# Performance work log

Hardware: AMD Instinct MI355X
Metric: run time of the kernel (lower is better)

## Reference

```python
import jax, jax.numpy as jnp
import numpy as np

IN_F = 128
OUT_F = 128
SCALE = float(np.sqrt(OUT_F))

def swish(x):
    return x * jax.nn.sigmoid(x)

def setup_inputs() -> dict:
    key = jax.random.key(0)
    ks = jax.random.split(key, 10)
    B, A = 4, 4096
    s = 1.0 / np.sqrt(IN_F)
    return {
        "x": jax.random.normal(ks[0], (B, A, IN_F), dtype=jnp.float32),
        "connectivity": jax.random.normal(ks[1], (B, A, A), dtype=jnp.float32),
        "Wq": jax.random.uniform(ks[2], (IN_F, OUT_F), jnp.float32, -s, s),
        "Wk": jax.random.uniform(ks[3], (IN_F, OUT_F), jnp.float32, -s, s),
        "Wv": jax.random.uniform(ks[4], (IN_F, OUT_F), jnp.float32, -s, s),
        "W1": jax.random.uniform(ks[5], (OUT_F, OUT_F), jnp.float32, -s, s),
        "b1": jnp.zeros((OUT_F,), jnp.float32),
        "W2": jax.random.uniform(ks[6], (OUT_F, OUT_F), jnp.float32, -s, s),
        "b2": jnp.zeros((OUT_F,), jnp.float32),
        "gamma": jnp.ones((OUT_F,), jnp.float32),
        "beta": jnp.zeros((OUT_F,), jnp.float32),
    }

def reference(x, connectivity, Wq, Wk, Wv, W1, b1, W2, b2, gamma, beta):
    # Q,K,V projections (no bias): [B,A,D]
    Q = jnp.einsum('bah,hd->bad', x, Wq)
    K = jnp.einsum('bah,hd->bad', x, Wk)
    V = jnp.einsum('bah,hd->bad', x, Wv)
    # dense all-pairs scores with additive connectivity bias: [B,A,A]
    scores = jnp.einsum('bqd,bkd->bqk', Q, K) / SCALE + connectivity
    alpha = jax.nn.softmax(scores, axis=-1)
    # dropout p=0.0 / eval mode -> identity
    H = jnp.einsum('bqk,bkd->bqd', alpha, V)
    # Swish-MLP tail
    h = swish(H)
    h = h @ W1 + b1
    h = swish(h)
    h = h @ W2 + b2
    # LayerNorm over last dim (eps=1e-5 as torch default)
    mu = jnp.mean(h, axis=-1, keepdims=True)
    var = jnp.var(h, axis=-1, keepdims=True)
    return (h - mu) * jax.lax.rsqrt(var + 1e-5) * gamma + beta
```

## Files before the change

### kernel.cpp

```cpp
#include <hip/hip_runtime.h>

#define L2E 1.44269504088896340736f
#define INV_SCALE 0.08838834764831845f

typedef _Float16 half8 __attribute__((ext_vector_type(8)));
typedef _Float16 half4 __attribute__((ext_vector_type(4)));
typedef float f32x4 __attribute__((ext_vector_type(4)));

__device__ __forceinline__ float exp2_fast(float x) {
#if __has_builtin(__builtin_amdgcn_exp2f)
  return __builtin_amdgcn_exp2f(x);
#else
  return exp2f(x);
#endif
}

__device__ __forceinline__ f32x4 mfma16(half8 a, half8 b, f32x4 c) {
  return __builtin_amdgcn_mfma_f32_16x16x32_f16(a, b, c, 0, 0, 0);
}

__device__ __forceinline__ void gload16(const void* g, void* l) {
  __builtin_amdgcn_global_load_lds(
      (const __attribute__((address_space(1))) void*)g,
      (__attribute__((address_space(3))) void*)l, 16, 0, 0);
}

__device__ __forceinline__ float swish_f(float v) {
  return v / (1.f + exp2_fast(-L2E * v));
}

template <int CTRL>
__device__ __forceinline__ float dppmov(float x) {
  int xi = __builtin_bit_cast(int, x);
  int r = __builtin_amdgcn_update_dpp(xi, xi, CTRL, 0xf, 0xf, false);
  return __builtin_bit_cast(float, r);
}
__device__ __forceinline__ float red16_sum(float x) {
  x += dppmov<0xB1>(x);
  x += dppmov<0x4E>(x);
  x += dppmov<0x141>(x);
  x += dppmov<0x140>(x);
  return x;
}

__global__ __launch_bounds__(256) void prep_kernel(
    const float* __restrict__ Wq, const float* __restrict__ Wk,
    const float* __restrict__ Wv, const float* __restrict__ W1,
    const float* __restrict__ W2, _Float16* __restrict__ Wf) {
  const int g = blockIdx.x * 256 + threadIdx.x;
  const int mat = g >> 11, rem = g & 2047;
  const int f = rem >> 6, lane = rem & 63;
  const int n = (f >> 2) * 16 + (lane & 15);
  const int k0 = (f & 3) * 32 + (lane >> 4) * 8;
  const float* W = (mat == 0) ? Wq : (mat == 1) ? Wk : (mat == 2) ? Wv
                   : (mat == 3) ? W1 : W2;
  half8 h;
#pragma unroll
  for (int j = 0; j < 8; ++j) h[j] = (_Float16)W[(k0 + j) * 128 + n];
  *(half8*)(Wf + (size_t)g * 8) = h;
}

__global__ __launch_bounds__(256) void kv_kernel(
    const float* __restrict__ x, const _Float16* __restrict__ Wf,
    _Float16* __restrict__ Kg, _Float16* __restrict__ Vg) {
  __shared__ __align__(16) _Float16 sc[64 * 136];
  const int tid = threadIdx.x;
  const int w = tid >> 6, lane = tid & 63;
  const int n16 = lane & 15, quad = lane >> 4;
  const int blk = blockIdx.x;

  half8 xf[4];
  {
    const float* xr = x + (size_t)(blk * 64 + w * 16 + n16) * 128 + quad * 8;
#pragma unroll
    for (int kc = 0; kc < 4; ++kc) {
      float4 a = *(const float4*)(xr + kc * 32);
      float4 b = *(const float4*)(xr + kc * 32 + 4);
      half8 h;
      h[0] = (_Float16)a.x; h[1] = (_Float16)a.y;
      h[2] = (_Float16)a.z; h[3] = (_Float16)a.w;
      h[4] = (_Float16)b.x; h[5] = (_Float16)b.y;
      h[6] = (_Float16)b.z; h[7] = (_Float16)b.w;
      xf[kc] = h;
    }
  }

  for (int mat = 0; mat < 2; ++mat) {
    f32x4 acc[8];
#pragma unroll
    for (int ct = 0; ct < 8; ++ct) acc[ct] = f32x4{0.f, 0.f, 0.f, 0.f};
#pragma unroll
    for (int ct = 0; ct < 8; ++ct)
#pragma unroll
      for (int kc = 0; kc < 4; ++kc) {
        half8 wf = *(const half8*)(Wf +
            ((size_t)((mat + 1) * 32 + ct * 4 + kc) * 64 + lane) * 8);
        acc[ct] = mfma16(xf[kc], wf, acc[ct]);
      }
#pragma unroll
    for (int ct = 0; ct < 8; ++ct)
#pragma unroll
      for (int r = 0; r < 4; ++r)
        sc[(w * 16 + quad * 4 + r) * 136 + ct * 16 + n16] = (_Float16)acc[ct][r];
    __syncthreads();

    if (mat == 0) {
#pragma unroll
      for (int i = 0; i < 4; ++i) {
        const int c = tid + 256 * i;
        const int ln = c & 63, kc = (c >> 6) & 3, ct = (c >> 8) & 1, tl = (c >> 9) & 1;
        half8 v = *(const half8*)&sc[(tl * 32 + ct * 16 + (ln & 15)) * 136 +
                                     kc * 32 + (ln >> 4) * 8];
        *(half8*)(Kg + ((((size_t)(blk * 2 + tl)) * 2 + ct) * 4 + kc) * 512 + ln * 8) = v;
      }
    } else {
#pragma unroll
      for (int i = 0; i < 4; ++i) {
        const int c = tid + 256 * i;
        const int ln = c & 63, dt = (c >> 6) & 7, tl = (c >> 9) & 1;
        const int q2 = ln >> 4, nn = ln & 15;
        half8 v;
#pragma unroll
        for (int j = 0; j < 8; ++j)
          v[j] = sc[(tl * 32 + q2 * 8 + j) * 136 + dt * 16 + nn];
        *(half8*)(Vg + (((size_t)(blk * 2 + tl)) * 8 + dt) * 512 + ln * 8) = v;
      }
    }
    __syncthreads();
  }
}

template <int NW>
__global__ __launch_bounds__(NW * 64) void flash_kernel(
    const float* __restrict__ x, const float* __restrict__ conn,
    const _Float16* __restrict__ Wf,
    const _Float16* __restrict__ Kg, const _Float16* __restrict__ Vg,
    _Float16* __restrict__ Og, float2* __restrict__ Ml,
    int nsplit, int nt) {
  __shared__ __align__(16) _Float16 kb[2][4096];
  __shared__ __align__(16) _Float16 vb[2][4096];
  __shared__ __align__(16) _Float16 pb[NW][656];
  __shared__ __align__(16) float alb[NW][16];

  const int tid = threadIdx.x, w = tid >> 6, lane = tid & 63;
  const int n16 = lane & 15, quad = lane >> 4;
  const int bid = blockIdx.x;
  int batch, sk, rg;
  if (nsplit == 4) {
    batch = bid & 3; sk = (bid >> 2) & 3; rg = bid >> 4;
  } else if (nsplit == 2) {
    batch = bid & 3; sk = (bid >> 2) & 1; rg = bid >> 3;
  } else {
    batch = bid & 3; sk = 0; rg = bid >> 2;
  }
  const int rt_g = batch * 256 + rg * NW + w;
  const int t0 = sk * nt;
  const int rowb = rg * (NW * 16) + w * 16 + n16;

  _Float16* scratch = (w < 2) ? &kb[w][0] : &vb[w - 2][0];

  half8 qf[4];
  {
    half8 xf[4];
    const float* xr = x + ((size_t)batch * 4096 + rowb) * 128 + quad * 8;
#pragma unroll
    for (int kc = 0; kc < 4; ++kc) {
      float4 a = *(const float4*)(xr + kc * 32);
      float4 b = *(const float4*)(xr + kc * 32 + 4);
      half8 h;
      h[0] = (_Float16)a.x; h[1] = (_Float16)a.y;
      h[2] = (_Float16)a.z; h[3] = (_Float16)a.w;
      h[4] = (_Float16)b.x; h[5] = (_Float16)b.y;
      h[6] = (_Float16)b.z; h[7] = (_Float16)b.w;
      xf[kc] = h;
    }
    _Float16* tw = scratch;
#pragma unroll
    for (int ct = 0; ct < 8; ++ct) {
      f32x4 aq = f32x4{0.f, 0.f, 0.f, 0.f};
#pragma unroll
      for (int kc = 0; kc < 4; ++kc) {
        half8 wf = *(const half8*)(Wf + ((size_t)(ct * 4 + kc) * 64 + lane) * 8);
        aq = mfma16(xf[kc], wf, aq);
      }
#pragma unroll
      for (int r = 0; r < 4; ++r)
        tw[(quad * 4 + r) * 136 + ct * 16 + n16] = (_Float16)aq[r];
    }
#pragma unroll
    for (int kc = 0; kc < 4; ++kc)
      qf[kc] = *(const half8*)(tw + n16 * 136 + kc * 32 + quad * 8);
  }
  __syncthreads();

  const _Float16* kp = Kg + (size_t)batch * 524288 + (size_t)t0 * 4096 + tid * 8;
  const _Float16* vp = Vg + (size_t)batch * 524288 + (size_t)t0 * 4096 + tid * 8;
  const float* cp = conn + (size_t)batch * 16777216 + (size_t)rowb * 4096 +
                    (size_t)t0 * 32 + quad * 4;
  const int wbase = (tid & ~63) * 8;
  constexpr int NC = 8 / NW;
  constexpr int PP = 2 * NC + 2;

  auto stage = [&](int t, int buf) {
    const _Float16* ks = kp + (size_t)t * 4096;
    const _Float16* vs = vp + (size_t)t * 4096;
#pragma unroll
    for (int c = 0; c < NC; ++c) {
      gload16(ks + c * (NW * 512), &kb[buf][c * (NW * 512) + wbase]);
      gload16(vs + c * (NW * 512), &vb[buf][c * (NW * 512) + wbase]);
    }
  };
  auto ldconn = [&](int i, float4* cr) {
    const float* c0 = cp + (size_t)i * 32;
    cr[0] = *(const float4*)c0;
    cr[1] = *(const float4*)(c0 + 16);
  };

  f32x4 o[8];
#pragma unroll
  for (int dt = 0; dt < 8; ++dt) o[dt] = f32x4{0.f, 0.f, 0.f, 0.f};
  float m_i = -__builtin_inff();
  float l_i = 0.f;

  auto compute = [&](int buf, const float4* cc) {
    f32x4 s0 = f32x4{0.f, 0.f, 0.f, 0.f};
    f32x4 s1 = f32x4{0.f, 0.f, 0.f, 0.f};
    const _Float16* kc_ = kb[buf];
    __builtin_amdgcn_s_setprio(1);
#pragma unroll
    for (int kc = 0; kc < 4; ++kc) {
      half8 kf0 = *(const half8*)&kc_[kc * 512 + lane * 8];
      half8 kf1 = *(const half8*)&kc_[(4 + kc) * 512 + lane * 8];
      s0 = mfma16(kf0, qf[kc], s0);
      s1 = mfma16(kf1, qf[kc], s1);
    }
    __builtin_amdgcn_s_setprio(0);
    float pr[8];
#pragma unroll
    for (int r = 0; r < 4; ++r) {
      pr[r] = fmaf(s0[r], INV_SCALE, cc[0][r]);
      pr[4 + r] = fmaf(s1[r], INV_SCALE, cc[1][r]);
    }
    float mx = pr[0];
#pragma unroll
    for (int c = 1; c < 8; ++c) mx = fmaxf(mx, pr[c]);
    mx = fmaxf(mx, __shfl_xor(mx, 16, 64));
    mx = fmaxf(mx, __shfl_xor(mx, 32, 64));
    if (__any(mx > m_i)) {
      const float mn = fmaxf(m_i, mx);
      const float al = exp2_fast((m_i - mn) * L2E);
      m_i = mn;
      l_i *= al;
      if (quad == 0) alb[w][n16] = al;
      const float4 av = *(const float4*)&alb[w][quad * 4];
#pragma unroll
      for (int dt = 0; dt < 8; ++dt)
#pragma unroll
        for (int r = 0; r < 4; ++r) o[dt][r] *= av[r];
    }
    const float nm = -m_i * L2E;
#pragma unroll
    for (int c = 0; c < 8; ++c) pr[c] = exp2_fast(fmaf(pr[c], L2E, nm));
    float sm = pr[0];
#pragma unroll
    for (int c = 1; c < 8; ++c) sm += pr[c];
    sm += __shfl_xor(sm, 16, 64);
    sm += __shfl_xor(sm, 32, 64);
    l_i += sm;
    _Float16* pw = pb[w];
    half4 p0, p1;
#pragma unroll
    for (int r = 0; r < 4; ++r) {
      p0[r] = (_Float16)pr[r];
      p1[r] = (_Float16)pr[4 + r];
    }
    *(half4*)(pw + n16 * 40 + quad * 4) = p0;
    *(half4*)(pw + n16 * 40 + 16 + quad * 4) = p1;
    half8 pf = *(const half8*)(pw + n16 * 40 + quad * 8);
    const _Float16* vc = vb[buf];
    __builtin_amdgcn_s_setprio(1);
#pragma unroll
    for (int dt = 0; dt < 8; ++dt) {
      half8 vf = *(const half8*)&vc[dt * 512 + lane * 8];
      o[dt] = mfma16(pf, vf, o[dt]);
    }
    __builtin_amdgcn_s_setprio(0);
  };

  float4 ca[2], cb[2];
  stage(0, 0);
  ldconn(0, ca);
  stage(1, 1);
  ldconn(1, cb);

#pragma unroll 1
  for (int t = 0; t < nt; t += 2) {
    asm volatile("s_waitcnt vmcnt(%0)" ::"n"(PP));
    __builtin_amdgcn_sched_barrier(0);
    __builtin_amdgcn_s_barrier();
    __builtin_amdgcn_sched_barrier(0);
    compute(0, ca);
    if (t + 2 < nt) {
      __builtin_amdgcn_sched_barrier(0);
      __builtin_amdgcn_s_barrier();
      stage(t + 2, 0);
      ldconn(t + 2, ca);
    }
    if (t + 2 < nt) {
      asm volatile("s_waitcnt vmcnt(%0)" ::"n"(PP));
    } else {
      asm volatile("s_waitcnt vmcnt(0)");
    }
    __builtin_amdgcn_sched_barrier(0);
    __builtin_amdgcn_s_barrier();
    __builtin_amdgcn_sched_barrier(0);
    compute(1, cb);
    if (t + 3 < nt) {
      __builtin_amdgcn_sched_barrier(0);
      __builtin_amdgcn_s_barrier();
      stage(t + 3, 1);
      ldconn(t + 3, cb);
    }
  }
  __builtin_amdgcn_sched_barrier(0);
  __builtin_amdgcn_s_barrier();

  if (quad == 0) alb[w][n16] = l_i;
  const float4 lv = *(const float4*)&alb[w][quad * 4];
  float il[4];
#pragma unroll
  for (int r = 0; r < 4; ++r) il[r] = 1.f / lv[r];
  _Float16* tw = scratch;
#pragma unroll
  for (int dt = 0; dt < 8; ++dt)
#pragma unroll
    for (int r = 0; r < 4; ++r)
      tw[(quad * 4 + r) * 136 + dt * 16 + n16] = (_Float16)(o[dt][r] * il[r]);
  _Float16* ob = Og + ((size_t)(sk * 1024 + rt_g) * 4) * 512;
#pragma unroll
  for (int kc = 0; kc < 4; ++kc) {
    half8 of = *(const half8*)(tw + n16 * 136 + kc * 32 + quad * 8);
    *(half8*)(ob + kc * 512 + lane * 8) = of;
  }
  if (quad == 0)
    Ml[sk * 16384 + rt_g * 16 + n16] = make_float2(m_i, l_i);
}

__global__ __launch_bounds__(256) void mlp_kernel(
    const _Float16* __restrict__ Og, const float2* __restrict__ Ml,
    const _Float16* __restrict__ Wf,
    const float* __restrict__ b1, const float* __restrict__ b2,
    const float* __restrict__ gamma, const float* __restrict__ beta,
    float* __restrict__ out, int nsplit) {
  __shared__ __align__(16) _Float16 hb[4][2176];
  const int tid = threadIdx.x, w = tid >> 6, lane = tid & 63;
  const int n16 = lane & 15, quad = lane >> 4;
  const int rt_g = blockIdx.x * 4 + w;

  float2 ml[4];
  float m = -__builtin_inff();
  for (int s = 0; s < nsplit; ++s) {
    ml[s] = Ml[s * 16384 + rt_g * 16 + n16];
    m = fmaxf(m, ml[s].x);
  }
  float wgt[4], wsum = 0.f;
  for (int s = 0; s < nsplit; ++s) {
    wgt[s] = ml[s].y * exp2_fast((ml[s].x - m) * L2E);
    wsum += wgt[s];
  }
  const float inv = 1.f / wsum;

  half8 hf[4];
#pragma unroll
  for (int kc = 0; kc < 4; ++kc) {
    float hv[8] = {0, 0, 0, 0, 0, 0, 0, 0};
    for (int s = 0; s < nsplit; ++s) {
      half8 ofr = *(const half8*)(Og +
          ((size_t)(s * 1024 + rt_g) * 4 + kc) * 512 + lane * 8);
#pragma unroll
      for (int j = 0; j < 8; ++j) hv[j] += wgt[s] * (float)ofr[j];
    }
    half8 h;
#pragma unroll
    for (int j = 0; j < 8; ++j) h[j] = (_Float16)swish_f(hv[j] * inv);
    hf[kc] = h;
  }

  float b1v[8], b2v[8], gv[8], bv[8];
#pragma unroll
  for (int ct = 0; ct < 8; ++ct) {
    b1v[ct] = b1[ct * 16 + n16];
    b2v[ct] = b2[ct * 16 + n16];
    gv[ct] = gamma[ct * 16 + n16];
    bv[ct] = beta[ct * 16 + n16];
  }

  f32x4 acc[8];
#pragma unroll
  for (int ct = 0; ct < 8; ++ct) acc[ct] = f32x4{0.f, 0.f, 0.f, 0.f};
#pragma unroll
  for (int ct = 0; ct < 8; ++ct)
#pragma unroll
    for (int kc = 0; kc < 4; ++kc) {
      half8 wf = *(const half8*)(Wf +
          ((size_t)(3 * 32 + ct * 4 + kc) * 64 + lane) * 8);
      acc[ct] = mfma16(hf[kc], wf, acc[ct]);
    }
  _Float16* hw = hb[w];
#pragma unroll
  for (int ct = 0; ct < 8; ++ct)
#pragma unroll
    for (int r = 0; r < 4; ++r)
      hw[(quad * 4 + r) * 136 + ct * 16 + n16] =
          (_Float16)swish_f(acc[ct][r] + b1v[ct]);
  half8 h1f[4];
#pragma unroll
  for (int kc = 0; kc < 4; ++kc)
    h1f[kc] = *(const half8*)(hw + n16 * 136 + kc * 32 + quad * 8);

#pragma unroll
  for (int ct = 0; ct < 8; ++ct) acc[ct] = f32x4{0.f, 0.f, 0.f, 0.f};
#pragma unroll
  for (int ct = 0; ct < 8; ++ct)
#pragma unroll
    for (int kc = 0; kc < 4; ++kc) {
      half8 wf = *(const half8*)(Wf +
          ((size_t)(4 * 32 + ct * 4 + kc) * 64 + lane) * 8);
      acc[ct] = mfma16(h1f[kc], wf, acc[ct]);
    }
  float hx[8][4];
  float sm[4] = {0, 0, 0, 0}, ss[4] = {0, 0, 0, 0};
#pragma unroll
  for (int ct = 0; ct < 8; ++ct)
#pragma unroll
    for (int r = 0; r < 4; ++r) {
      const float v = acc[ct][r] + b2v[ct];
      hx[ct][r] = v;
      sm[r] += v;
      ss[r] += v * v;
    }
#pragma unroll
  for (int r = 0; r < 4; ++r) {
    sm[r] = red16_sum(sm[r]);
    ss[r] = red16_sum(ss[r]);
  }
#pragma unroll
  for (int r = 0; r < 4; ++r) {
    const float mu = sm[r] * (1.f / 128.f);
    const float var = ss[r] * (1.f / 128.f) - mu * mu;
    const float rstd = rsqrtf(var + 1e-5f);
    const size_t row = (size_t)rt_g * 16 + quad * 4 + r;
#pragma unroll
    for (int ct = 0; ct < 8; ++ct)
      out[row * 128 + ct * 16 + n16] = (hx[ct][r] - mu) * rstd * gv[ct] + bv[ct];
  }
}

extern "C" void kernel_launch(void* const* d_in, const int* in_sizes, int n_in,
                              void* d_out, int out_size, void* d_ws,
                              size_t ws_size, hipStream_t stream) {
  const float* x     = (const float*)d_in[0];
  const float* conn  = (const float*)d_in[1];
  const float* Wq    = (const float*)d_in[2];
  const float* Wk    = (const float*)d_in[3];
  const float* Wv    = (const float*)d_in[4];
  const float* W1    = (const float*)d_in[5];
  const float* b1    = (const float*)d_in[6];
  const float* W2    = (const float*)d_in[7];
  const float* b2    = (const float*)d_in[8];
  const float* gamma = (const float*)d_in[9];
  const float* beta  = (const float*)d_in[10];
  float* out = (float*)d_out;

  const size_t baseElems = (size_t)81920 + 2 * 2097152;
  const size_t need4 =
      (baseElems + 4 * 2097152) * 2 + 4 * 16384 * sizeof(float2);
  const size_t need2 =
      (baseElems + 2 * 2097152) * 2 + 2 * 16384 * sizeof(float2);
  const int nsplit = (ws_size >= need4) ? 4 : (ws_size >= need2) ? 2 : 1;
  const int nt = 128 / nsplit;

  _Float16* Wf = (_Float16*)d_ws;
  _Float16* Kg = Wf + 81920;
  _Float16* Vg = Kg + 2097152;
  _Float16* Og = Vg + 2097152;
  float2* Ml = (float2*)(Og + (size_t)2097152 * nsplit);

  prep_kernel<<<40, 256, 0, stream>>>(Wq, Wk, Wv, W1, W2, Wf);
  kv_kernel<<<256, 256, 0, stream>>>(x, Wf, Kg, Vg);
  if (nsplit == 4) {
    flash_kernel<4><<<1024, 256, 0, stream>>>(x, conn, Wf, Kg, Vg, Og, Ml,
                                              nsplit, nt);
  } else if (nsplit == 2) {
    flash_kernel<2><<<1024, 128, 0, stream>>>(x, conn, Wf, Kg, Vg, Og, Ml,
                                              nsplit, nt);
  } else {
    flash_kernel<2><<<512, 128, 0, stream>>>(x, conn, Wf, Kg, Vg, Og, Ml,
                                             nsplit, nt);
  }
  mlp_kernel<<<256, 256, 0, stream>>>(Og, Ml, Wf, b1, b2, gamma, beta, out,
                                      nsplit);
}
```

Baseline: 477.3 us.

## Prefetch connectivity bias in 4-tile groups two groups ahead in flash loop

The main flash-attention loop now loads the connectivity bias for four key tiles at once, two groups (eight tiles) ahead, and uses separate high and low vmcnt wait thresholds instead of fetching two floats4 per tile just one tile ahead. The goal is to hide the latency of the large fp32 connectivity stream behind more in-flight work. The launch bounds also add a minimum of 3 blocks per SM. The cost is more registers for the connectivity buffers (16 float4) and a more complex epilogue, which assumes nt is a multiple of 4 and at least 8.

```diff
diff --git a/kernel.cpp b/kernel.cpp
--- a/kernel.cpp
+++ b/kernel.cpp
@@ -131,7 +131,7 @@
 }
 
 template <int NW>
-__global__ __launch_bounds__(NW * 64) void flash_kernel(
+__global__ __launch_bounds__(NW * 64, 3) void flash_kernel(
     const float* __restrict__ x, const float* __restrict__ conn,
     const _Float16* __restrict__ Wf,
     const _Float16* __restrict__ Kg, const _Float16* __restrict__ Vg,
@@ -199,7 +199,9 @@
                     (size_t)t0 * 32 + quad * 4;
   const int wbase = (tid & ~63) * 8;
   constexpr int NC = 8 / NW;
-  constexpr int PP = 2 * NC + 2;
+  constexpr int ST = 2 * NC;
+  constexpr int W_HI = ST + 8;
+  constexpr int W_LO = ST;
 
   auto stage = [&](int t, int buf) {
     const _Float16* ks = kp + (size_t)t * 4096;
@@ -210,10 +212,10 @@
       gload16(vs + c * (NW * 512), &vb[buf][c * (NW * 512) + wbase]);
     }
   };
-  auto ldconn = [&](int i, float4* cr) {
-    const float* c0 = cp + (size_t)i * 32;
-    cr[0] = *(const float4*)c0;
-    cr[1] = *(const float4*)(c0 + 16);
+  auto ldconn_group = [&](int g, float4* cr) {
+    const float* c0 = cp + (size_t)g * 128;
+#pragma unroll
+    for (int j = 0; j < 8; ++j) cr[j] = *(const float4*)(c0 + j * 16);
   };
 
   f32x4 o[8];
@@ -287,43 +289,65 @@
     __builtin_amdgcn_s_setprio(0);
   };
 
-  float4 ca[2], cb[2];
+  const int NG = nt >> 2;
+  float4 cA[8], cB[8];
+
+  ldconn_group(0, cA);
   stage(0, 0);
-  ldconn(0, ca);
   stage(1, 1);
-  ldconn(1, cb);
+  ldconn_group(1, cB);
+
+  auto group_body = [&](int g, float4* C) {
+    const int tb = g * 4;
+#pragma unroll
+    for (int p = 0; p < 4; ++p) {
+      if (p < 2) {
+        asm volatile("s_waitcnt vmcnt(%0)" ::"n"(W_HI));
+      } else {
+        asm volatile("s_waitcnt vmcnt(%0)" ::"n"(W_LO));
+      }
+      __builtin_amdgcn_sched_barrier(0);
+      __builtin_amdgcn_s_barrier();
+      __builtin_amdgcn_sched_barrier(0);
+      compute(p & 1, &C[2 * p]);
+      __builtin_amdgcn_sched_barrier(0);
+      __builtin_amdgcn_s_barrier();
+      __builtin_amdgcn_sched_barrier(0);
+      stage(tb + p + 2, p & 1);
+      __builtin_amdgcn_sched_barrier(0);
+    }
+    if (g + 2 < NG) ldconn_group(g + 2, C);
+    __builtin_amdgcn_sched_barrier(0);
+  };
 
 #pragma unroll 1
-  for (int t = 0; t < nt; t += 2) {
-    asm volatile("s_waitcnt vmcnt(%0)" ::"n"(PP));
-    __builtin_amdgcn_sched_barrier(0);
-    __builtin_amdgcn_s_barrier();
-    __builtin_amdgcn_sched_barrier(0);
-    compute(0, ca);
-    if (t + 2 < nt) {
+  for (int g = 0; g + 3 < NG; g += 2) {
+    group_body(g, cA);
+    group_body(g + 1, cB);
+  }
+  group_body(NG - 2, cA);
+
+  {
+#pragma unroll
+    for (int p = 0; p < 4; ++p) {
+      if (p < 3) {
+        asm volatile("s_waitcnt vmcnt(%0)" ::"n"(W_LO));
+      } else {
+        asm volatile("s_waitcnt vmcnt(0)");
+      }
       __builtin_amdgcn_sched_barrier(0);
       __builtin_amdgcn_s_barrier();
-      stage(t + 2, 0);
-      ldconn(t + 2, ca);
-    }
-    if (t + 2 < nt) {
-      asm volatile("s_waitcnt vmcnt(%0)" ::"n"(PP));
-    } else {
-      asm volatile("s_waitcnt vmcnt(0)");
-    }
-    __builtin_amdgcn_sched_barrier(0);
-    __builtin_amdgcn_s_barrier();
-    __builtin_amdgcn_sched_barrier(0);
-    compute(1, cb);
-    if (t + 3 < nt) {
+      __builtin_amdgcn_sched_barrier(0);
+      compute(p & 1, &cB[2 * p]);
       __builtin_amdgcn_sched_barrier(0);
       __builtin_amdgcn_s_barrier();
-      stage(t + 3, 1);
-      ldconn(t + 3, cb);
-    }
-  }
-  __builtin_amdgcn_sched_barrier(0);
-  __builtin_amdgcn_s_barrier();
+      __builtin_amdgcn_sched_barrier(0);
+      if (p < 2) {
+        stage((NG - 1) * 4 + p + 2, p & 1);
+        __builtin_amdgcn_sched_barrier(0);
+      }
+    }
+  }
 
   if (quad == 0) alb[w][n16] = l_i;
   const float4 lv = *(const float4*)&alb[w][quad * 4];
```

Result: faster. 438.9 us (-8.1%).
